# Performance work log

Hardware: AMD Instinct MI355X
Metric: run time of the kernel (lower is better)

The kernel has to match this reference:

```python
import jax, jax.numpy as jnp
import numpy as np

PATCH = 16  # conv kernel size == stride


def _patch_embed(im, W, b):
    # im: (B, C, H, W) NCHW; W: (hidden, C, s, s); returns (B, h, w, hidden)
    out = jax.lax.conv_general_dilated(
        im, W, window_strides=(PATCH, PATCH), padding='VALID',
        dimension_numbers=('NCHW', 'OIHW', 'NCHW'))
    out = out + b[None, :, None, None]
    return jnp.transpose(out, (0, 2, 3, 1))  # (B, h, w, hidden)


def setup_inputs() -> dict:
    key = jax.random.key(0)
    k1, k2, k3, k4 = jax.random.split(key, 4)
    B, C, H, Wd = 64, 3, 224, 224
    hidden = 384
    x = jax.random.normal(k1, (B, C, H, Wd), dtype=jnp.float32)
    y = jax.random.normal(k2, (B, C, H, Wd), dtype=jnp.float32)
    fan_in = C * PATCH * PATCH
    bound = 1.0 / np.sqrt(fan_in)
    W = jax.random.uniform(k3, (hidden, C, PATCH, PATCH), dtype=jnp.float32,
                           minval=-bound, maxval=bound)
    b = jax.random.uniform(k4, (hidden,), dtype=jnp.float32,
                           minval=-bound, maxval=bound)
    return {'x': x, 'y': y, 'W': W, 'b': b}


def reference(x, y, W, b):
    B = x.shape[0]
    xp = _patch_embed(x, W, b)  # (B, h, w, C)
    yp = _patch_embed(y, W, b)  # (B, h, w, C)
    h, w = xp.shape[1], xp.shape[2]
    logp = jax.nn.log_softmax(xp, axis=-1)          # (B, h, w, C)
    q = jax.lax.stop_gradient(jax.nn.softmax(yp, axis=-1))  # detached targets
    # CE[i, j] = mean over (h, w) of -(q_j * logp_i).sum(-1)
    # Faithful factorization of the (B, B, h, w, C) broadcast in the original.
    CE = -jnp.einsum('ihwc,jhwc->ij', logp, q) / (h * w)  # (B, B)
    close = jnp.trace(CE) / B
    far = (CE.sum() - jnp.trace(CE)) / (B * B - B)
    return close / far
```

## Files before the change

### kernel.cpp

```cpp
#include <hip/hip_runtime.h>

#define HID   384
#define K_PE  768
#define IMGST 150528
#define POS   196

typedef unsigned short ushort_t;
using f32x4  = __attribute__((ext_vector_type(4))) float;
using short8 = __attribute__((ext_vector_type(8))) short;

typedef unsigned __attribute__((address_space(1))) u32_g;
typedef unsigned __attribute__((address_space(3))) u32_s;

__device__ __forceinline__ void glds16(const void* g, void* l) {
    __builtin_amdgcn_global_load_lds((const u32_g*)g, (u32_s*)l, 16, 0, 0);
}

__device__ __forceinline__ unsigned bfpack(float lo, float hi) {
    union { float f; unsigned u; } a, b; a.f = lo; b.f = hi;
    unsigned ra = (a.u + 0x7fffu + ((a.u >> 16) & 1u)) >> 16;
    unsigned rb = (b.u + 0x7fffu + ((b.u >> 16) & 1u)) & 0xffff0000u;
    return ra | rb;
}

__global__ __launch_bounds__(256) void pack(
    const float* __restrict__ x, const float* __restrict__ y,
    const float* __restrict__ W, ushort_t* __restrict__ Wfrag,
    ushort_t* __restrict__ imx, ushort_t* __restrict__ imy,
    float* __restrict__ scal, int* __restrict__ pcnt,
    float* __restrict__ Lp, float* __restrict__ Qp) {
    const int b   = blockIdx.x;
    const int tid = threadIdx.x;

    if (b >= 896) {
        const int t = (b - 896) * 256 + tid;
        if (t < 16)  scal[t] = 0.f;
        if (t < POS) pcnt[t] = 0;
        for (int i = t; i < POS * HID; i += 36864) { Lp[i] = 0.f; Qp[i] = 0.f; }
        const int n  = t / 96;
        const int ko = t - n * 96;
        const float4 a  = *(const float4*)(W + (size_t)n * K_PE + ko * 8);
        const float4 bb = *(const float4*)(W + (size_t)n * K_PE + ko * 8 + 4);
        uint4 pq;
        pq.x = bfpack(a.x, a.y);  pq.y = bfpack(a.z, a.w);
        pq.z = bfpack(bb.x, bb.y); pq.w = bfpack(bb.z, bb.w);
        const int nt    = n >> 4;
        const int kc    = ko >> 2;
        const int lanew = (ko & 3) * 16 + (n & 15);
        ((uint4*)Wfrag)[(nt * 24 + kc) * 64 + lanew] = pq;
        return;
    }

    const int pi  = b >> 6;
    const int img = b & 63;
    __shared__ __align__(16) ushort_t L[2][48 * 232];

    const float* bx = x + (size_t)img * IMGST + pi * 3584;
    const float* by = y + (size_t)img * IMGST + pi * 3584;

    for (int i = tid; i < 2688; i += 256) {
        const int row = i / 56;
        const int c4  = i - row * 56;
        const int c   = row >> 4, r = row & 15;
        const size_t so = (size_t)c * 50176 + r * 224 + c4 * 4;
        const float4 fx = *(const float4*)(bx + so);
        const float4 fy = *(const float4*)(by + so);
        uint2 px, py;
        px.x = bfpack(fx.x, fx.y); px.y = bfpack(fx.z, fx.w);
        py.x = bfpack(fy.x, fy.y); py.y = bfpack(fy.z, fy.w);
        *(uint2*)&L[0][row * 232 + c4 * 4] = px;
        *(uint2*)&L[1][row * 232 + c4 * 4] = py;
    }
    __syncthreads();

    for (int u = tid; u < 1344; u += 256) {
        const int pj  = u / 96;
        const int oc  = u - pj * 96;
        const int kbi = oc >> 3, o = oc & 7;
        const int k0  = oc * 8;
        const int c   = k0 >> 8, kh = (k0 >> 4) & 15, kw0 = k0 & 15;
        const int loff = (c * 16 + kh) * 232 + pj * 16 + kw0;
        const uint4 vx = *(const uint4*)&L[0][loff];
        const uint4 vy = *(const uint4*)&L[1][loff];
        const size_t d = ((size_t)((pi * 14 + pj) * 12 + kbi) * 64 + img) * 64 + o * 8;
        *(uint4*)&imx[d] = vx;
        *(uint4*)&imy[d] = vy;
    }
}

__global__ __launch_bounds__(256, 3) void pe2(
    const ushort_t* __restrict__ imx, const ushort_t* __restrict__ imy,
    const ushort_t* __restrict__ Wfrag, const float* __restrict__ bias,
    float* __restrict__ scal, int* __restrict__ pcnt,
    float* __restrict__ Lp, float* __restrict__ Qp, float* __restrict__ out) {
    const int blk  = blockIdx.x;
    const int p    = blk >> 1;
    const int half = blk & 1;

    __shared__ __align__(16) ushort_t As[2][4096];
    __shared__ float Smx[4][32], Ssx[4][32], Smy[4][32], Ssy[4][32];
    __shared__ float sT[4];
    __shared__ int lastp;

    const int tid  = threadIdx.x;
    const int wave = tid >> 6;
    const int lane = tid & 63;
    const int lm   = lane & 15;
    const int lq   = lane >> 4;

    const int simg = wave * 8 + (lane >> 3);
    const int so   = (lane & 7) ^ ((lane >> 3) & 7);
    const size_t sbyte = (size_t)p * 98304 +
                         ((size_t)(half * 32 + simg)) * 128 + so * 16;
    const char* gx = (const char*)imx + sbyte;
    const char* gy = (const char*)imy + sbyte;

    int ard[2][2];
#pragma unroll
    for (int ks = 0; ks < 2; ++ks)
#pragma unroll
        for (int mi = 0; mi < 2; ++mi)
            ard[ks][mi] = (mi * 16 + lm) * 64 + (((ks * 4 + lq) ^ (lm & 7)) * 8);

    const ushort_t* bbase = Wfrag + (size_t)lane * 8;

    f32x4 accx[2][6] = {};
    f32x4 accy[2][6] = {};

#define STAGE(KB, BUF)                                       \
    {                                                        \
        glds16(gx + (size_t)(KB) * 8192, &As[BUF][wave * 512]);        \
        glds16(gy + (size_t)(KB) * 8192, &As[BUF][2048 + wave * 512]); \
    }

    STAGE(0, 0)
    __syncthreads();

    for (int kbi = 0; kbi < 12; ++kbi) {
        const int cur = kbi & 1;
#pragma unroll
        for (int ks = 0; ks < 2; ++ks) {
            short8 bfr[6];
#pragma unroll
            for (int ni = 0; ni < 6; ++ni)
                bfr[ni] = *(const short8*)(bbase +
                          (size_t)(((wave * 6 + ni) * 24 + kbi * 2 + ks) * 64) * 8);
            if (ks == 0 && kbi < 11) STAGE(kbi + 1, cur ^ 1)
            short8 afx[2], afy[2];
#pragma unroll
            for (int mi = 0; mi < 2; ++mi) {
                afx[mi] = *(const short8*)&As[cur][ard[ks][mi]];
                afy[mi] = *(const short8*)&As[cur][2048 + ard[ks][mi]];
            }
#pragma unroll
            for (int mi = 0; mi < 2; ++mi)
#pragma unroll
                for (int ni = 0; ni < 6; ++ni) {
                    accx[mi][ni] = __builtin_amdgcn_mfma_f32_16x16x32_bf16(
                        afx[mi], bfr[ni], accx[mi][ni], 0, 0, 0);
                    accy[mi][ni] = __builtin_amdgcn_mfma_f32_16x16x32_bf16(
                        afy[mi], bfr[ni], accy[mi][ni], 0, 0, 0);
                }
        }
        __syncthreads();
    }
#undef STAGE

#pragma unroll
    for (int ni = 0; ni < 6; ++ni) {
        const float bv = bias[wave * 96 + ni * 16 + lm];
#pragma unroll
        for (int mi = 0; mi < 2; ++mi)
#pragma unroll
            for (int r = 0; r < 4; ++r) {
                accx[mi][ni][r] += bv;
                accy[mi][ni][r] += bv;
            }
    }

    float mx[2][4], my_[2][4];
#pragma unroll
    for (int mi = 0; mi < 2; ++mi)
#pragma unroll
        for (int r = 0; r < 4; ++r) {
            float a = accx[mi][0][r], bb = accy[mi][0][r];
#pragma unroll
            for (int ni = 1; ni < 6; ++ni) {
                a  = fmaxf(a,  accx[mi][ni][r]);
                bb = fmaxf(bb, accy[mi][ni][r]);
            }
            mx[mi][r] = a; my_[mi][r] = bb;
        }
#pragma unroll
    for (int off = 1; off < 16; off <<= 1)
#pragma unroll
        for (int mi = 0; mi < 2; ++mi)
#pragma unroll
            for (int r = 0; r < 4; ++r) {
                mx[mi][r]  = fmaxf(mx[mi][r],  __shfl_xor(mx[mi][r],  off));
                my_[mi][r] = fmaxf(my_[mi][r], __shfl_xor(my_[mi][r], off));
            }
    if (lm == 0)
#pragma unroll
        for (int mi = 0; mi < 2; ++mi)
#pragma unroll
            for (int r = 0; r < 4; ++r) {
                Smx[wave][mi * 16 + lq * 4 + r] = mx[mi][r];
                Smy[wave][mi * 16 + lq * 4 + r] = my_[mi][r];
            }
    __syncthreads();
#pragma unroll
    for (int mi = 0; mi < 2; ++mi)
#pragma unroll
        for (int r = 0; r < 4; ++r) {
            const int row = mi * 16 + lq * 4 + r;
            mx[mi][r]  = fmaxf(fmaxf(Smx[0][row], Smx[1][row]),
                               fmaxf(Smx[2][row], Smx[3][row]));
            my_[mi][r] = fmaxf(fmaxf(Smy[0][row], Smy[1][row]),
                               fmaxf(Smy[2][row], Smy[3][row]));
        }

    float sx[2][4], sy[2][4];
#pragma unroll
    for (int mi = 0; mi < 2; ++mi)
#pragma unroll
        for (int r = 0; r < 4; ++r) {
            float a = 0.f, bb = 0.f;
#pragma unroll
            for (int ni = 0; ni < 6; ++ni) {
                a  += __expf(accx[mi][ni][r] - mx[mi][r]);
                bb += __expf(accy[mi][ni][r] - my_[mi][r]);
            }
            sx[mi][r] = a; sy[mi][r] = bb;
        }
#pragma unroll
    for (int off = 1; off < 16; off <<= 1)
#pragma unroll
        for (int mi = 0; mi < 2; ++mi)
#pragma unroll
            for (int r = 0; r < 4; ++r) {
                sx[mi][r] += __shfl_xor(sx[mi][r], off);
                sy[mi][r] += __shfl_xor(sy[mi][r], off);
            }
    if (lm == 0)
#pragma unroll
        for (int mi = 0; mi < 2; ++mi)
#pragma unroll
            for (int r = 0; r < 4; ++r) {
                Ssx[wave][mi * 16 + lq * 4 + r] = sx[mi][r];
                Ssy[wave][mi * 16 + lq * 4 + r] = sy[mi][r];
            }
    __syncthreads();
    float shx[2][4], invy[2][4];
#pragma unroll
    for (int mi = 0; mi < 2; ++mi)
#pragma unroll
        for (int r = 0; r < 4; ++r) {
            const int row = mi * 16 + lq * 4 + r;
            const float ssx = Ssx[0][row] + Ssx[1][row] + Ssx[2][row] + Ssx[3][row];
            const float ssy = Ssy[0][row] + Ssy[1][row] + Ssy[2][row] + Ssy[3][row];
            shx[mi][r]  = mx[mi][r] + __logf(ssx);
            invy[mi][r] = 1.f / ssy;
        }

    float T = 0.f;
    float cL[6], cQ[6];
#pragma unroll
    for (int ni = 0; ni < 6; ++ni) { cL[ni] = 0.f; cQ[ni] = 0.f; }
#pragma unroll
    for (int mi = 0; mi < 2; ++mi)
#pragma unroll
        for (int r = 0; r < 4; ++r) {
            const float sh  = shx[mi][r];
            const float m   = my_[mi][r];
            const float inv = invy[mi][r];
#pragma unroll
            for (int ni = 0; ni < 6; ++ni) {
                const float lp = accx[mi][ni][r] - sh;
                const float qv = __expf(accy[mi][ni][r] - m) * inv;
                T += lp * qv;
                cL[ni] += lp;
                cQ[ni] += qv;
            }
        }
#pragma unroll
    for (int ni = 0; ni < 6; ++ni) {
        cL[ni] += __shfl_xor(cL[ni], 16); cL[ni] += __shfl_xor(cL[ni], 32);
        cQ[ni] += __shfl_xor(cQ[ni], 16); cQ[ni] += __shfl_xor(cQ[ni], 32);
    }
    if (lq == 0)
#pragma unroll
        for (int ni = 0; ni < 6; ++ni) {
            atomicAdd(&Lp[p * HID + wave * 96 + ni * 16 + lm], cL[ni]);
            atomicAdd(&Qp[p * HID + wave * 96 + ni * 16 + lm], cQ[ni]);
        }
#pragma unroll
    for (int off = 32; off > 0; off >>= 1) T += __shfl_xor(T, off);
    if (lane == 0) sT[wave] = T;
    __syncthreads();
    if (tid == 0) {
        atomicAdd(&scal[0], sT[0] + sT[1] + sT[2] + sT[3]);
        __threadfence();
        const int old = atomicAdd(&pcnt[p], 1);
        lastp = (old == 1);
    }
    __syncthreads();

    if (lastp) {
        float s = 0.f;
        for (int c = tid; c < HID; c += 256) {
            const float Lv = atomicAdd(&Lp[p * HID + c], 0.f);
            const float Qv = atomicAdd(&Qp[p * HID + c], 0.f);
            s += Lv * Qv;
        }
#pragma unroll
        for (int off = 32; off > 0; off >>= 1) s += __shfl_xor(s, off);
        if (lane == 0) sT[wave] = s;
        __syncthreads();
        if (tid == 0) atomicAdd(&scal[1], sT[0] + sT[1] + sT[2] + sT[3]);
    }

    if (tid == 0) {
        __threadfence();
        const int g = atomicAdd((int*)&scal[3], 1);
        if (g == (int)gridDim.x - 1) {
            const float Tt = atomicAdd(&scal[0], 0.f);
            const float St = atomicAdd(&scal[1], 0.f);
            out[0] = 63.f * Tt / (St - Tt);
        }
    }
}

extern "C" void kernel_launch(void* const* d_in, const int* in_sizes, int n_in,
                              void* d_out, int out_size, void* d_ws, size_t ws_size,
                              hipStream_t stream) {
    const float* x = (const float*)d_in[0];
    const float* y = (const float*)d_in[1];
    const float* W = (const float*)d_in[2];
    const float* b = (const float*)d_in[3];
    float* out = (float*)d_out;

    char* ws = (char*)d_ws;
    float*    scal  = (float*)ws;
    int*      pcnt  = (int*)(ws + 1024);
    ushort_t* Wfrag = (ushort_t*)(ws + 2048);
    float*    Lp    = (float*)(ws + 591872);
    float*    Qp    = (float*)(ws + 892928);
    ushort_t* imx   = (ushort_t*)(ws + 1196032);
    ushort_t* imy   = (ushort_t*)(ws + 20463616);

    pack<<<1040, 256, 0, stream>>>(x, y, W, Wfrag, imx, imy, scal, pcnt, Lp, Qp);
    pe2<<<392, 256, 0, stream>>>(imx, imy, Wfrag, b, scal, pcnt, Lp, Qp, out);
}
```

Before: 155.2 us.

## Split pack and patch-embed GEMM blocks finer to raise CU occupancy

The pack kernel now gives each block a single tensor (x or y) instead of both, doubling the block count and halving LDS use. The GEMM/softmax kernel splits each patch position into four 16-image blocks instead of two 32-image blocks, giving 784 blocks with smaller LDS and accumulator footprints and a launch bound of 4 blocks per CU. The aim is better spread across the MI355X compute units and more latency hiding. In exchange, each weight fragment is reloaded by twice as many blocks, each MFMA A-fragment is reused less, and there are more atomics per position.

```diff
diff --git a/kernel.cpp b/kernel.cpp
--- a/kernel.cpp
+++ b/kernel.cpp
@@ -32,8 +32,8 @@
     const int b   = blockIdx.x;
     const int tid = threadIdx.x;
 
-    if (b >= 896) {
-        const int t = (b - 896) * 256 + tid;
+    if (b >= 1792) {
+        const int t = (b - 1792) * 256 + tid;
         if (t < 16)  scal[t] = 0.f;
         if (t < POS) pcnt[t] = 0;
         for (int i = t; i < POS * HID; i += 36864) { Lp[i] = 0.f; Qp[i] = 0.f; }
@@ -42,7 +42,7 @@
         const float4 a  = *(const float4*)(W + (size_t)n * K_PE + ko * 8);
         const float4 bb = *(const float4*)(W + (size_t)n * K_PE + ko * 8 + 4);
         uint4 pq;
-        pq.x = bfpack(a.x, a.y);  pq.y = bfpack(a.z, a.w);
+        pq.x = bfpack(a.x, a.y);   pq.y = bfpack(a.z, a.w);
         pq.z = bfpack(bb.x, bb.y); pq.w = bfpack(bb.z, bb.w);
         const int nt    = n >> 4;
         const int kc    = ko >> 2;
@@ -51,28 +51,26 @@
         return;
     }
 
-    const int pi  = b >> 6;
-    const int img = b & 63;
-    __shared__ __align__(16) ushort_t L[2][48 * 232];
-
-    const float* bx = x + (size_t)img * IMGST + pi * 3584;
-    const float* by = y + (size_t)img * IMGST + pi * 3584;
+    const int pi  = b >> 7;
+    const int img = (b >> 1) & 63;
+    const int tn  = b & 1;
+    __shared__ __align__(16) ushort_t L[48 * 232];
+
+    const float* bp = (tn ? y : x) + (size_t)img * IMGST + pi * 3584;
 
     for (int i = tid; i < 2688; i += 256) {
         const int row = i / 56;
         const int c4  = i - row * 56;
         const int c   = row >> 4, r = row & 15;
         const size_t so = (size_t)c * 50176 + r * 224 + c4 * 4;
-        const float4 fx = *(const float4*)(bx + so);
-        const float4 fy = *(const float4*)(by + so);
-        uint2 px, py;
-        px.x = bfpack(fx.x, fx.y); px.y = bfpack(fx.z, fx.w);
-        py.x = bfpack(fy.x, fy.y); py.y = bfpack(fy.z, fy.w);
-        *(uint2*)&L[0][row * 232 + c4 * 4] = px;
-        *(uint2*)&L[1][row * 232 + c4 * 4] = py;
-    }
-    __syncthreads();
-
+        const float4 f = *(const float4*)(bp + so);
+        uint2 px;
+        px.x = bfpack(f.x, f.y); px.y = bfpack(f.z, f.w);
+        *(uint2*)&L[row * 232 + c4 * 4] = px;
+    }
+    __syncthreads();
+
+    ushort_t* __restrict__ im = tn ? imy : imx;
     for (int u = tid; u < 1344; u += 256) {
         const int pj  = u / 96;
         const int oc  = u - pj * 96;
@@ -80,25 +78,23 @@
         const int k0  = oc * 8;
         const int c   = k0 >> 8, kh = (k0 >> 4) & 15, kw0 = k0 & 15;
         const int loff = (c * 16 + kh) * 232 + pj * 16 + kw0;
-        const uint4 vx = *(const uint4*)&L[0][loff];
-        const uint4 vy = *(const uint4*)&L[1][loff];
+        const uint4 v = *(const uint4*)&L[loff];
         const size_t d = ((size_t)((pi * 14 + pj) * 12 + kbi) * 64 + img) * 64 + o * 8;
-        *(uint4*)&imx[d] = vx;
-        *(uint4*)&imy[d] = vy;
-    }
-}
-
-__global__ __launch_bounds__(256, 3) void pe2(
+        *(uint4*)&im[d] = v;
+    }
+}
+
+__global__ __launch_bounds__(256, 4) void pe3(
     const ushort_t* __restrict__ imx, const ushort_t* __restrict__ imy,
     const ushort_t* __restrict__ Wfrag, const float* __restrict__ bias,
     float* __restrict__ scal, int* __restrict__ pcnt,
     float* __restrict__ Lp, float* __restrict__ Qp, float* __restrict__ out) {
-    const int blk  = blockIdx.x;
-    const int p    = blk >> 1;
-    const int half = blk & 1;
-
-    __shared__ __align__(16) ushort_t As[2][4096];
-    __shared__ float Smx[4][32], Ssx[4][32], Smy[4][32], Ssy[4][32];
+    const int blk = blockIdx.x;
+    const int p   = blk >> 2;
+    const int sub = blk & 3;
+
+    __shared__ __align__(16) ushort_t As[2][2048];
+    __shared__ float Smx[4][16], Ssx[4][16], Smy[4][16], Ssy[4][16];
     __shared__ float sT[4];
     __shared__ int lastp;
 
@@ -108,30 +104,25 @@
     const int lm   = lane & 15;
     const int lq   = lane >> 4;
 
-    const int simg = wave * 8 + (lane >> 3);
-    const int so   = (lane & 7) ^ ((lane >> 3) & 7);
-    const size_t sbyte = (size_t)p * 98304 +
-                         ((size_t)(half * 32 + simg)) * 128 + so * 16;
-    const char* gx = (const char*)imx + sbyte;
-    const char* gy = (const char*)imy + sbyte;
-
-    int ard[2][2];
+    const int t_   = tid >> 7;
+    const int srow = (tid & 127) >> 3;
+    const int s_   = lane & 7;
+    const int o_   = s_ ^ (srow & 7);
+    const char* gsrc = (const char*)(t_ ? imy : imx) +
+        (size_t)p * 98304 + (size_t)(sub * 16 + srow) * 128 + o_ * 16;
+    const int wbase = wave * 512;
+
+    int ard[2];
 #pragma unroll
     for (int ks = 0; ks < 2; ++ks)
-#pragma unroll
-        for (int mi = 0; mi < 2; ++mi)
-            ard[ks][mi] = (mi * 16 + lm) * 64 + (((ks * 4 + lq) ^ (lm & 7)) * 8);
+        ard[ks] = lm * 64 + (((ks * 4 + lq) ^ (lm & 7)) * 8);
 
     const ushort_t* bbase = Wfrag + (size_t)lane * 8;
 
-    f32x4 accx[2][6] = {};
-    f32x4 accy[2][6] = {};
-
-#define STAGE(KB, BUF)                                       \
-    {                                                        \
-        glds16(gx + (size_t)(KB) * 8192, &As[BUF][wave * 512]);        \
-        glds16(gy + (size_t)(KB) * 8192, &As[BUF][2048 + wave * 512]); \
-    }
+    f32x4 accx[6] = {};
+    f32x4 accy[6] = {};
+
+#define STAGE(KB, BUF) glds16(gsrc + (size_t)(KB) * 8192, &As[BUF][wbase]);
 
     STAGE(0, 0)
     __syncthreads();
@@ -146,21 +137,15 @@
                 bfr[ni] = *(const short8*)(bbase +
                           (size_t)(((wave * 6 + ni) * 24 + kbi * 2 + ks) * 64) * 8);
             if (ks == 0 && kbi < 11) STAGE(kbi + 1, cur ^ 1)
-            short8 afx[2], afy[2];
-#pragma unroll
-            for (int mi = 0; mi < 2; ++mi) {
-                afx[mi] = *(const short8*)&As[cur][ard[ks][mi]];
-                afy[mi] = *(const short8*)&As[cur][2048 + ard[ks][mi]];
+            const short8 afx = *(const short8*)&As[cur][ard[ks]];
+            const short8 afy = *(const short8*)&As[cur][1024 + ard[ks]];
+#pragma unroll
+            for (int ni = 0; ni < 6; ++ni) {
+                accx[ni] = __builtin_amdgcn_mfma_f32_16x16x32_bf16(
+                    afx, bfr[ni], accx[ni], 0, 0, 0);
+                accy[ni] = __builtin_amdgcn_mfma_f32_16x16x32_bf16(
+                    afy, bfr[ni], accy[ni], 0, 0, 0);
             }
-#pragma unroll
-            for (int mi = 0; mi < 2; ++mi)
-#pragma unroll
-                for (int ni = 0; ni < 6; ++ni) {
-                    accx[mi][ni] = __builtin_amdgcn_mfma_f32_16x16x32_bf16(
-                        afx[mi], bfr[ni], accx[mi][ni], 0, 0, 0);
-                    accy[mi][ni] = __builtin_amdgcn_mfma_f32_16x16x32_bf16(
-                        afy[mi], bfr[ni], accy[mi][ni], 0, 0, 0);
-                }
         }
         __syncthreads();
     }
@@ -170,119 +155,99 @@
     for (int ni = 0; ni < 6; ++ni) {
         const float bv = bias[wave * 96 + ni * 16 + lm];
 #pragma unroll
-        for (int mi = 0; mi < 2; ++mi)
-#pragma unroll
-            for (int r = 0; r < 4; ++r) {
-                accx[mi][ni][r] += bv;
-                accy[mi][ni][r] += bv;
-            }
-    }
-
-    float mx[2][4], my_[2][4];
-#pragma unroll
-    for (int mi = 0; mi < 2; ++mi)
-#pragma unroll
-        for (int r = 0; r < 4; ++r) {
-            float a = accx[mi][0][r], bb = accy[mi][0][r];
-#pragma unroll
-            for (int ni = 1; ni < 6; ++ni) {
-                a  = fmaxf(a,  accx[mi][ni][r]);
-                bb = fmaxf(bb, accy[mi][ni][r]);
-            }
-            mx[mi][r] = a; my_[mi][r] = bb;
-        }
+        for (int r = 0; r < 4; ++r) {
+            accx[ni][r] += bv;
+            accy[ni][r] += bv;
+        }
+    }
+
+    float mx[4], my_[4];
+#pragma unroll
+    for (int r = 0; r < 4; ++r) {
+        float a = accx[0][r], bb = accy[0][r];
+#pragma unroll
+        for (int ni = 1; ni < 6; ++ni) {
+            a  = fmaxf(a,  accx[ni][r]);
+            bb = fmaxf(bb, accy[ni][r]);
+        }
+        mx[r] = a; my_[r] = bb;
+    }
 #pragma unroll
     for (int off = 1; off < 16; off <<= 1)
 #pragma unroll
-        for (int mi = 0; mi < 2; ++mi)
-#pragma unroll
-            for (int r = 0; r < 4; ++r) {
-                mx[mi][r]  = fmaxf(mx[mi][r],  __shfl_xor(mx[mi][r],  off));
-                my_[mi][r] = fmaxf(my_[mi][r], __shfl_xor(my_[mi][r], off));
-            }
+        for (int r = 0; r < 4; ++r) {
+            mx[r]  = fmaxf(mx[r],  __shfl_xor(mx[r],  off));
+            my_[r] = fmaxf(my_[r], __shfl_xor(my_[r], off));
+        }
     if (lm == 0)
 #pragma unroll
-        for (int mi = 0; mi < 2; ++mi)
-#pragma unroll
-            for (int r = 0; r < 4; ++r) {
-                Smx[wave][mi * 16 + lq * 4 + r] = mx[mi][r];
-                Smy[wave][mi * 16 + lq * 4 + r] = my_[mi][r];
-            }
-    __syncthreads();
-#pragma unroll
-    for (int mi = 0; mi < 2; ++mi)
-#pragma unroll
-        for (int r = 0; r < 4; ++r) {
-            const int row = mi * 16 + lq * 4 + r;
-            mx[mi][r]  = fmaxf(fmaxf(Smx[0][row], Smx[1][row]),
-                               fmaxf(Smx[2][row], Smx[3][row]));
-            my_[mi][r] = fmaxf(fmaxf(Smy[0][row], Smy[1][row]),
-                               fmaxf(Smy[2][row], Smy[3][row]));
-        }
-
-    float sx[2][4], sy[2][4];
-#pragma unroll
-    for (int mi = 0; mi < 2; ++mi)
-#pragma unroll
-        for (int r = 0; r < 4; ++r) {
-            float a = 0.f, bb = 0.f;
-#pragma unroll
-            for (int ni = 0; ni < 6; ++ni) {
-                a  += __expf(accx[mi][ni][r] - mx[mi][r]);
-                bb += __expf(accy[mi][ni][r] - my_[mi][r]);
-            }
-            sx[mi][r] = a; sy[mi][r] = bb;
-        }
+        for (int r = 0; r < 4; ++r) {
+            Smx[wave][lq * 4 + r] = mx[r];
+            Smy[wave][lq * 4 + r] = my_[r];
+        }
+    __syncthreads();
+#pragma unroll
+    for (int r = 0; r < 4; ++r) {
+        const int row = lq * 4 + r;
+        mx[r]  = fmaxf(fmaxf(Smx[0][row], Smx[1][row]),
+                       fmaxf(Smx[2][row], Smx[3][row]));
+        my_[r] = fmaxf(fmaxf(Smy[0][row], Smy[1][row]),
+                       fmaxf(Smy[2][row], Smy[3][row]));
+    }
+
+    float sx[4], sy[4];
+#pragma unroll
+    for (int r = 0; r < 4; ++r) {
+        float a = 0.f, bb = 0.f;
+#pragma unroll
+        for (int ni = 0; ni < 6; ++ni) {
+            a  += __expf(accx[ni][r] - mx[r]);
+            bb += __expf(accy[ni][r] - my_[r]);
+        }
+        sx[r] = a; sy[r] = bb;
+    }
 #pragma unroll
     for (int off = 1; off < 16; off <<= 1)
 #pragma unroll
-        for (int mi = 0; mi < 2; ++mi)
-#pragma unroll
-            for (int r = 0; r < 4; ++r) {
-                sx[mi][r] += __shfl_xor(sx[mi][r], off);
-                sy[mi][r] += __shfl_xor(sy[mi][r], off);
-            }
+        for (int r = 0; r < 4; ++r) {
+            sx[r] += __shfl_xor(sx[r], off);
+            sy[r] += __shfl_xor(sy[r], off);
+        }
     if (lm == 0)
 #pragma unroll
-        for (int mi = 0; mi < 2; ++mi)
-#pragma unroll
-            for (int r = 0; r < 4; ++r) {
-                Ssx[wave][mi * 16 + lq * 4 + r] = sx[mi][r];
-                Ssy[wave][mi * 16 + lq * 4 + r] = sy[mi][r];
-            }
-    __syncthreads();
-    float shx[2][4], invy[2][4];
-#pragma unroll
-    for (int mi = 0; mi < 2; ++mi)
-#pragma unroll
-        for (int r = 0; r < 4; ++r) {
-            const int row = mi * 16 + lq * 4 + r;
-            const float ssx = Ssx[0][row] + Ssx[1][row] + Ssx[2][row] + Ssx[3][row];
-            const float ssy = Ssy[0][row] + Ssy[1][row] + Ssy[2][row] + Ssy[3][row];
-            shx[mi][r]  = mx[mi][r] + __logf(ssx);
-            invy[mi][r] = 1.f / ssy;
-        }
+        for (int r = 0; r < 4; ++r) {
+            Ssx[wave][lq * 4 + r] = sx[r];
+            Ssy[wave][lq * 4 + r] = sy[r];
+        }
+    __syncthreads();
+    float shx[4], invy[4];
+#pragma unroll
+    for (int r = 0; r < 4; ++r) {
+        const int row = lq * 4 + r;
+        const float ssx = Ssx[0][row] + Ssx[1][row] + Ssx[2][row] + Ssx[3][row];
+        const float ssy = Ssy[0][row] + Ssy[1][row] + Ssy[2][row] + Ssy[3][row];
+        shx[r]  = mx[r] + __logf(ssx);
+        invy[r] = 1.f / ssy;
+    }
 
     float T = 0.f;
     float cL[6], cQ[6];
 #pragma unroll
     for (int ni = 0; ni < 6; ++ni) { cL[ni] = 0.f; cQ[ni] = 0.f; }
 #pragma unroll
-    for (int mi = 0; mi < 2; ++mi)
-#pragma unroll
-        for (int r = 0; r < 4; ++r) {
-            const float sh  = shx[mi][r];
-            const float m   = my_[mi][r];
-            const float inv = invy[mi][r];
-#pragma unroll
-            for (int ni = 0; ni < 6; ++ni) {
-                const float lp = accx[mi][ni][r] - sh;
-                const float qv = __expf(accy[mi][ni][r] - m) * inv;
-                T += lp * qv;
-                cL[ni] += lp;
-                cQ[ni] += qv;
-            }
-        }
+    for (int r = 0; r < 4; ++r) {
+        const float sh  = shx[r];
+        const float m   = my_[r];
+        const float inv = invy[r];
+#pragma unroll
+        for (int ni = 0; ni < 6; ++ni) {
+            const float lp = accx[ni][r] - sh;
+            const float qv = __expf(accy[ni][r] - m) * inv;
+            T += lp * qv;
+            cL[ni] += lp;
+            cQ[ni] += qv;
+        }
+    }
 #pragma unroll
     for (int ni = 0; ni < 6; ++ni) {
         cL[ni] += __shfl_xor(cL[ni], 16); cL[ni] += __shfl_xor(cL[ni], 32);
@@ -302,7 +267,7 @@
         atomicAdd(&scal[0], sT[0] + sT[1] + sT[2] + sT[3]);
         __threadfence();
         const int old = atomicAdd(&pcnt[p], 1);
-        lastp = (old == 1);
+        lastp = (old == 3);
     }
     __syncthreads();
 
@@ -349,6 +314,6 @@
     ushort_t* imx   = (ushort_t*)(ws + 1196032);
     ushort_t* imy   = (ushort_t*)(ws + 20463616);
 
-    pack<<<1040, 256, 0, stream>>>(x, y, W, Wfrag, imx, imy, scal, pcnt, Lp, Qp);
-    pe2<<<392, 256, 0, stream>>>(imx, imy, Wfrag, b, scal, pcnt, Lp, Qp, out);
-}
+    pack<<<1936, 256, 0, stream>>>(x, y, W, Wfrag, imx, imy, scal, pcnt, Lp, Qp);
+    pe3<<<784, 256, 0, stream>>>(imx, imy, Wfrag, b, scal, pcnt, Lp, Qp, out);
+}
```

Result: slower. 163.3 us (+5.2%).

## Fuse image im2col/bf16 conversion into GEMM and split column reduction into separate kernel

Applied to the files above, without the earlier changes.

Removes the separate pack kernel that wrote bf16 im2col copies of x and y to workspace. The GEMM kernel now reads fp32 pixels directly, converts them to bf16 and stages them in LDS with a register double buffer. Each block now handles 2 images by 14 patches for one patch row, with 28 of 32 M rows active. Per-position logp and q values are written to global memory instead of being accumulated with atomics, and a new fin kernel reduces them over images and finishes the scalar. This trades the im2col round trip and atomic contention for wasted MFMA rows, a larger L/Q write and read (about 19MB each), and an extra launch.

```diff
diff --git a/kernel.cpp b/kernel.cpp
--- a/kernel.cpp
+++ b/kernel.cpp
@@ -8,13 +8,6 @@
 typedef unsigned short ushort_t;
 using f32x4  = __attribute__((ext_vector_type(4))) float;
 using short8 = __attribute__((ext_vector_type(8))) short;
-
-typedef unsigned __attribute__((address_space(1))) u32_g;
-typedef unsigned __attribute__((address_space(3))) u32_s;
-
-__device__ __forceinline__ void glds16(const void* g, void* l) {
-    __builtin_amdgcn_global_load_lds((const u32_g*)g, (u32_s*)l, 16, 0, 0);
-}
 
 __device__ __forceinline__ unsigned bfpack(float lo, float hi) {
     union { float f; unsigned u; } a, b; a.f = lo; b.f = hi;
@@ -23,84 +16,35 @@
     return ra | rb;
 }
 
-__global__ __launch_bounds__(256) void pack(
+__global__ __launch_bounds__(256) void prep(const float* __restrict__ W,
+                                            ushort_t* __restrict__ Wfrag,
+                                            float* __restrict__ scal) {
+    const int t = blockIdx.x * 256 + threadIdx.x;
+    if (t < 4) scal[t] = 0.f;
+    const int n  = t / 96;
+    const int ko = t - n * 96;
+    const float4 a  = *(const float4*)(W + (size_t)n * K_PE + ko * 8);
+    const float4 bb = *(const float4*)(W + (size_t)n * K_PE + ko * 8 + 4);
+    uint4 pq;
+    pq.x = bfpack(a.x, a.y);   pq.y = bfpack(a.z, a.w);
+    pq.z = bfpack(bb.x, bb.y); pq.w = bfpack(bb.z, bb.w);
+    const int nt    = n >> 4;
+    const int kc    = ko >> 2;
+    const int lanew = (ko & 3) * 16 + (n & 15);
+    ((uint4*)Wfrag)[(nt * 24 + kc) * 64 + lanew] = pq;
+}
+
+__global__ __launch_bounds__(256, 2) void pef(
     const float* __restrict__ x, const float* __restrict__ y,
-    const float* __restrict__ W, ushort_t* __restrict__ Wfrag,
-    ushort_t* __restrict__ imx, ushort_t* __restrict__ imy,
-    float* __restrict__ scal, int* __restrict__ pcnt,
-    float* __restrict__ Lp, float* __restrict__ Qp) {
-    const int b   = blockIdx.x;
-    const int tid = threadIdx.x;
-
-    if (b >= 896) {
-        const int t = (b - 896) * 256 + tid;
-        if (t < 16)  scal[t] = 0.f;
-        if (t < POS) pcnt[t] = 0;
-        for (int i = t; i < POS * HID; i += 36864) { Lp[i] = 0.f; Qp[i] = 0.f; }
-        const int n  = t / 96;
-        const int ko = t - n * 96;
-        const float4 a  = *(const float4*)(W + (size_t)n * K_PE + ko * 8);
-        const float4 bb = *(const float4*)(W + (size_t)n * K_PE + ko * 8 + 4);
-        uint4 pq;
-        pq.x = bfpack(a.x, a.y);  pq.y = bfpack(a.z, a.w);
-        pq.z = bfpack(bb.x, bb.y); pq.w = bfpack(bb.z, bb.w);
-        const int nt    = n >> 4;
-        const int kc    = ko >> 2;
-        const int lanew = (ko & 3) * 16 + (n & 15);
-        ((uint4*)Wfrag)[(nt * 24 + kc) * 64 + lanew] = pq;
-        return;
-    }
-
-    const int pi  = b >> 6;
-    const int img = b & 63;
-    __shared__ __align__(16) ushort_t L[2][48 * 232];
-
-    const float* bx = x + (size_t)img * IMGST + pi * 3584;
-    const float* by = y + (size_t)img * IMGST + pi * 3584;
-
-    for (int i = tid; i < 2688; i += 256) {
-        const int row = i / 56;
-        const int c4  = i - row * 56;
-        const int c   = row >> 4, r = row & 15;
-        const size_t so = (size_t)c * 50176 + r * 224 + c4 * 4;
-        const float4 fx = *(const float4*)(bx + so);
-        const float4 fy = *(const float4*)(by + so);
-        uint2 px, py;
-        px.x = bfpack(fx.x, fx.y); px.y = bfpack(fx.z, fx.w);
-        py.x = bfpack(fy.x, fy.y); py.y = bfpack(fy.z, fy.w);
-        *(uint2*)&L[0][row * 232 + c4 * 4] = px;
-        *(uint2*)&L[1][row * 232 + c4 * 4] = py;
-    }
-    __syncthreads();
-
-    for (int u = tid; u < 1344; u += 256) {
-        const int pj  = u / 96;
-        const int oc  = u - pj * 96;
-        const int kbi = oc >> 3, o = oc & 7;
-        const int k0  = oc * 8;
-        const int c   = k0 >> 8, kh = (k0 >> 4) & 15, kw0 = k0 & 15;
-        const int loff = (c * 16 + kh) * 232 + pj * 16 + kw0;
-        const uint4 vx = *(const uint4*)&L[0][loff];
-        const uint4 vy = *(const uint4*)&L[1][loff];
-        const size_t d = ((size_t)((pi * 14 + pj) * 12 + kbi) * 64 + img) * 64 + o * 8;
-        *(uint4*)&imx[d] = vx;
-        *(uint4*)&imy[d] = vy;
-    }
-}
-
-__global__ __launch_bounds__(256, 3) void pe2(
-    const ushort_t* __restrict__ imx, const ushort_t* __restrict__ imy,
     const ushort_t* __restrict__ Wfrag, const float* __restrict__ bias,
-    float* __restrict__ scal, int* __restrict__ pcnt,
-    float* __restrict__ Lp, float* __restrict__ Qp, float* __restrict__ out) {
-    const int blk  = blockIdx.x;
-    const int p    = blk >> 1;
-    const int half = blk & 1;
-
-    __shared__ __align__(16) ushort_t As[2][4096];
+    float* __restrict__ scal, float* __restrict__ Lg, float* __restrict__ Qg) {
+    const int blk = blockIdx.x;
+    const int pi  = blk >> 5;
+    const int ig  = blk & 31;
+
+    __shared__ __align__(16) ushort_t As[2][1792];
     __shared__ float Smx[4][32], Ssx[4][32], Smy[4][32], Ssy[4][32];
     __shared__ float sT[4];
-    __shared__ int lastp;
 
     const int tid  = threadIdx.x;
     const int wave = tid >> 6;
@@ -108,63 +52,87 @@
     const int lm   = lane & 15;
     const int lq   = lane >> 4;
 
-    const int simg = wave * 8 + (lane >> 3);
-    const int so   = (lane & 7) ^ ((lane >> 3) & 7);
-    const size_t sbyte = (size_t)p * 98304 +
-                         ((size_t)(half * 32 + simg)) * 128 + so * 16;
-    const char* gx = (const char*)imx + sbyte;
-    const char* gy = (const char*)imy + sbyte;
+    const int rr   = tid >> 5;
+    const int sj   = tid & 31;
+    const int st   = rr >> 2;
+    const int simg = (rr >> 1) & 1;
+    const int skh  = rr & 1;
+    const int sq   = sj & 1;
+    const int spj  = sj >> 1;
+    const bool sact = sj < 28;
+    const float* srow = (st ? y : x) +
+        (size_t)(ig * 2 + simg) * IMGST + pi * 3584 + sj * 8;
+    const int aoff = (((skh * 2 + sq) * 2 + st) * 2 + simg) * 112 + spj * 8;
 
     int ard[2][2];
 #pragma unroll
-    for (int ks = 0; ks < 2; ++ks)
-#pragma unroll
-        for (int mi = 0; mi < 2; ++mi)
-            ard[ks][mi] = (mi * 16 + lm) * 64 + (((ks * 4 + lq) ^ (lm & 7)) * 8);
-
-    const ushort_t* bbase = Wfrag + (size_t)lane * 8;
+    for (int t = 0; t < 2; ++t)
+#pragma unroll
+        for (int mi = 0; mi < 2; ++mi) {
+            int m = mi * 16 + lm; if (m > 27) m = 27;
+            const int img = (m >= 14) ? 1 : 0;
+            const int pj  = m - img * 14;
+            ard[t][mi] = ((lq * 2 + t) * 2 + img) * 112 + pj * 8;
+        }
 
     f32x4 accx[2][6] = {};
     f32x4 accy[2][6] = {};
 
-#define STAGE(KB, BUF)                                       \
-    {                                                        \
-        glds16(gx + (size_t)(KB) * 8192, &As[BUF][wave * 512]);        \
-        glds16(gy + (size_t)(KB) * 8192, &As[BUF][2048 + wave * 512]); \
-    }
-
-    STAGE(0, 0)
-    __syncthreads();
-
-    for (int kbi = 0; kbi < 12; ++kbi) {
-        const int cur = kbi & 1;
-#pragma unroll
-        for (int ks = 0; ks < 2; ++ks) {
-            short8 bfr[6];
-#pragma unroll
-            for (int ni = 0; ni < 6; ++ni)
-                bfr[ni] = *(const short8*)(bbase +
-                          (size_t)(((wave * 6 + ni) * 24 + kbi * 2 + ks) * 64) * 8);
-            if (ks == 0 && kbi < 11) STAGE(kbi + 1, cur ^ 1)
-            short8 afx[2], afy[2];
-#pragma unroll
-            for (int mi = 0; mi < 2; ++mi) {
-                afx[mi] = *(const short8*)&As[cur][ard[ks][mi]];
-                afy[mi] = *(const short8*)&As[cur][2048 + ard[ks][mi]];
-            }
+    if (sact) {
+        const float4 f0 = *(const float4*)(srow + skh * 224);
+        const float4 f1 = *(const float4*)(srow + skh * 224 + 4);
+        uint4 px;
+        px.x = bfpack(f0.x, f0.y); px.y = bfpack(f0.z, f0.w);
+        px.z = bfpack(f1.x, f1.y); px.w = bfpack(f1.z, f1.w);
+        *(uint4*)&As[0][aoff] = px;
+    }
+    short8 bfr[6];
+#pragma unroll
+    for (int ni = 0; ni < 6; ++ni)
+        bfr[ni] = *(const short8*)(Wfrag +
+                  (size_t)(((wave * 6 + ni) * 24) * 64 + lane) * 8);
+    __syncthreads();
+
+#pragma unroll 2
+    for (int kk = 0; kk < 24; ++kk) {
+        const int cur = kk & 1;
+        const int kn  = (kk < 23) ? kk + 1 : 0;
+        const int off = (kn >> 3) * 50176 + ((kn & 7) * 2 + skh) * 224;
+        float4 f0{}, f1{};
+        if (sact) {
+            f0 = *(const float4*)(srow + off);
+            f1 = *(const float4*)(srow + off + 4);
+        }
+        short8 bfrn[6];
+#pragma unroll
+        for (int ni = 0; ni < 6; ++ni)
+            bfrn[ni] = *(const short8*)(Wfrag +
+                       (size_t)(((wave * 6 + ni) * 24 + kn) * 64 + lane) * 8);
+        short8 af[2][2];
+#pragma unroll
+        for (int t = 0; t < 2; ++t)
 #pragma unroll
             for (int mi = 0; mi < 2; ++mi)
-#pragma unroll
-                for (int ni = 0; ni < 6; ++ni) {
-                    accx[mi][ni] = __builtin_amdgcn_mfma_f32_16x16x32_bf16(
-                        afx[mi], bfr[ni], accx[mi][ni], 0, 0, 0);
-                    accy[mi][ni] = __builtin_amdgcn_mfma_f32_16x16x32_bf16(
-                        afy[mi], bfr[ni], accy[mi][ni], 0, 0, 0);
-                }
-        }
+                af[t][mi] = *(const short8*)&As[cur][ard[t][mi]];
+#pragma unroll
+        for (int mi = 0; mi < 2; ++mi)
+#pragma unroll
+            for (int ni = 0; ni < 6; ++ni) {
+                accx[mi][ni] = __builtin_amdgcn_mfma_f32_16x16x32_bf16(
+                    af[0][mi], bfr[ni], accx[mi][ni], 0, 0, 0);
+                accy[mi][ni] = __builtin_amdgcn_mfma_f32_16x16x32_bf16(
+                    af[1][mi], bfr[ni], accy[mi][ni], 0, 0, 0);
+            }
+        if (sact) {
+            uint4 px;
+            px.x = bfpack(f0.x, f0.y); px.y = bfpack(f0.z, f0.w);
+            px.z = bfpack(f1.x, f1.y); px.w = bfpack(f1.z, f1.w);
+            *(uint4*)&As[cur ^ 1][aoff] = px;
+        }
+#pragma unroll
+        for (int ni = 0; ni < 6; ++ni) bfr[ni] = bfrn[ni];
         __syncthreads();
     }
-#undef STAGE
 
 #pragma unroll
     for (int ni = 0; ni < 6; ++ni) {
@@ -264,69 +232,66 @@
         }
 
     float T = 0.f;
-    float cL[6], cQ[6];
-#pragma unroll
-    for (int ni = 0; ni < 6; ++ni) { cL[ni] = 0.f; cQ[ni] = 0.f; }
-#pragma unroll
-    for (int mi = 0; mi < 2; ++mi)
-#pragma unroll
-        for (int r = 0; r < 4; ++r) {
-            const float sh  = shx[mi][r];
-            const float m   = my_[mi][r];
-            const float inv = invy[mi][r];
-#pragma unroll
-            for (int ni = 0; ni < 6; ++ni) {
-                const float lp = accx[mi][ni][r] - sh;
-                const float qv = __expf(accy[mi][ni][r] - m) * inv;
-                T += lp * qv;
-                cL[ni] += lp;
-                cQ[ni] += qv;
-            }
-        }
-#pragma unroll
-    for (int ni = 0; ni < 6; ++ni) {
-        cL[ni] += __shfl_xor(cL[ni], 16); cL[ni] += __shfl_xor(cL[ni], 32);
-        cQ[ni] += __shfl_xor(cQ[ni], 16); cQ[ni] += __shfl_xor(cQ[ni], 32);
-    }
-    if (lq == 0)
-#pragma unroll
-        for (int ni = 0; ni < 6; ++ni) {
-            atomicAdd(&Lp[p * HID + wave * 96 + ni * 16 + lm], cL[ni]);
-            atomicAdd(&Qp[p * HID + wave * 96 + ni * 16 + lm], cQ[ni]);
+#pragma unroll
+    for (int mi = 0; mi < 2; ++mi)
+#pragma unroll
+        for (int r = 0; r < 4; ++r) {
+            const int m = mi * 16 + lq * 4 + r;
+            if (m < 28) {
+                const int img = (m >= 14) ? 1 : 0;
+                const int pj  = m - img * 14;
+                const size_t lb = ((size_t)(pi * 64 + ig * 2 + img) * 14 + pj) * 384
+                                  + wave * 96 + lm;
+                const float sh  = shx[mi][r];
+                const float mm  = my_[mi][r];
+                const float inv = invy[mi][r];
+#pragma unroll
+                for (int ni = 0; ni < 6; ++ni) {
+                    const float lp = accx[mi][ni][r] - sh;
+                    const float qv = __expf(accy[mi][ni][r] - mm) * inv;
+                    T += lp * qv;
+                    Lg[lb + ni * 16] = lp;
+                    Qg[lb + ni * 16] = qv;
+                }
+            }
         }
 #pragma unroll
     for (int off = 32; off > 0; off >>= 1) T += __shfl_xor(T, off);
     if (lane == 0) sT[wave] = T;
     __syncthreads();
-    if (tid == 0) {
-        atomicAdd(&scal[0], sT[0] + sT[1] + sT[2] + sT[3]);
+    if (tid == 0) atomicAdd(&scal[0], sT[0] + sT[1] + sT[2] + sT[3]);
+}
+
+__global__ __launch_bounds__(384) void fin(const float* __restrict__ Lg,
+                                           const float* __restrict__ Qg,
+                                           float* __restrict__ scal,
+                                           float* __restrict__ out) {
+    const int p  = blockIdx.x;
+    const int pi = p / 14;
+    const int pj = p - pi * 14;
+    const int c  = threadIdx.x;
+    float L = 0.f, Q = 0.f;
+#pragma unroll 4
+    for (int img = 0; img < 64; ++img) {
+        const size_t o = ((size_t)(pi * 64 + img) * 14 + pj) * 384 + c;
+        L += Lg[o];
+        Q += Qg[o];
+    }
+    float s = L * Q;
+#pragma unroll
+    for (int off = 32; off > 0; off >>= 1) s += __shfl_xor(s, off);
+    __shared__ float sw[6];
+    if ((c & 63) == 0) sw[c >> 6] = s;
+    __syncthreads();
+    if (c == 0) {
+        const float Sp = sw[0] + sw[1] + sw[2] + sw[3] + sw[4] + sw[5];
+        atomicAdd(&scal[1], Sp);
         __threadfence();
-        const int old = atomicAdd(&pcnt[p], 1);
-        lastp = (old == 1);
-    }
-    __syncthreads();
-
-    if (lastp) {
-        float s = 0.f;
-        for (int c = tid; c < HID; c += 256) {
-            const float Lv = atomicAdd(&Lp[p * HID + c], 0.f);
-            const float Qv = atomicAdd(&Qp[p * HID + c], 0.f);
-            s += Lv * Qv;
-        }
-#pragma unroll
-        for (int off = 32; off > 0; off >>= 1) s += __shfl_xor(s, off);
-        if (lane == 0) sT[wave] = s;
-        __syncthreads();
-        if (tid == 0) atomicAdd(&scal[1], sT[0] + sT[1] + sT[2] + sT[3]);
-    }
-
-    if (tid == 0) {
-        __threadfence();
-        const int g = atomicAdd((int*)&scal[3], 1);
-        if (g == (int)gridDim.x - 1) {
-            const float Tt = atomicAdd(&scal[0], 0.f);
-            const float St = atomicAdd(&scal[1], 0.f);
-            out[0] = 63.f * Tt / (St - Tt);
+        const int old = atomicAdd((int*)&scal[3], 1);
+        if (old == POS - 1) {
+            const float T = atomicAdd(&scal[0], 0.f);
+            const float S = atomicAdd(&scal[1], 0.f);
+            out[0] = 63.f * T / (S - T);
         }
     }
 }
@@ -342,13 +307,11 @@
 
     char* ws = (char*)d_ws;
     float*    scal  = (float*)ws;
-    int*      pcnt  = (int*)(ws + 1024);
-    ushort_t* Wfrag = (ushort_t*)(ws + 2048);
-    float*    Lp    = (float*)(ws + 591872);
-    float*    Qp    = (float*)(ws + 892928);
-    ushort_t* imx   = (ushort_t*)(ws + 1196032);
-    ushort_t* imy   = (ushort_t*)(ws + 20463616);
-
-    pack<<<1040, 256, 0, stream>>>(x, y, W, Wfrag, imx, imy, scal, pcnt, Lp, Qp);
-    pe2<<<392, 256, 0, stream>>>(imx, imy, Wfrag, b, scal, pcnt, Lp, Qp, out);
-}
+    ushort_t* Wfrag = (ushort_t*)(ws + 1024);
+    float*    Lg    = (float*)(ws + 590848);
+    float*    Qg    = (float*)(ws + 19858432);
+
+    prep<<<144, 256, 0, stream>>>(W, Wfrag, scal);
+    pef<<<448, 256, 0, stream>>>(x, y, Wfrag, b, scal, Lg, Qg);
+    fin<<<196, 384, 0, stream>>>(Lg, Qg, scal, out);
+}
```

Measured after the change: 151.0 us. 2.7% less time.
